# Performance work log

Measured on AMD Instinct MI355X. Metric: run time of the kernel, lower is better.

The kernel has to match this reference:

```python
import jax, jax.numpy as jnp
import numpy as np

TWO_PI = 2.0 * np.pi
EPS = 1e-6


def fourier_embed(x, W):
    # Gaussian Fourier features: x (B,L,1), W (1,F) -> (B,L,2F)
    p = TWO_PI * (x @ W)
    return jnp.concatenate([jnp.sin(p), jnp.cos(p)], axis=-1)


def phi(x, proj):
    # Stable positive softmax kernel (FAVOR+ eq. 7): exp(x W^T - |x|^2/2)/sqrt(m)
    m = proj.shape[0]
    xp = jnp.einsum('blhd,md->blhm', x, proj)
    h = 0.5 * jnp.sum(jnp.square(x), axis=-1, keepdims=True)
    return jnp.exp(xp - h) / jnp.sqrt(m)


def setup_inputs() -> dict:
    key = jax.random.key(0)
    kq, kk, kv, kqs, kks, kw, kp, ka = jax.random.split(key, 8)
    B, L, H, D, Dv = 4, 4096, 8, 64, 64
    M, S = 256, 64  # num_ortho_features, s_embd_dim
    return {
        'qs': jax.random.normal(kq, (B, L, H, D), jnp.float32),
        'ks': jax.random.normal(kk, (B, L, H, D), jnp.float32),
        'vs': jax.random.normal(kv, (B, L, H, Dv), jnp.float32),
        'qs_s': jax.random.uniform(kqs, (B, L, 1), jnp.float32),
        'ks_s': jax.random.uniform(kks, (B, L, 1), jnp.float32),
        'fourier_W': jax.random.normal(kw, (1, S // 2), jnp.float32),
        'qk_proj': jax.random.normal(kp, (M, D + S // H), jnp.float32),
        'a': jax.random.normal(ka, (1, 1, H, 1), jnp.float32),
    }


def reference(qs, ks, vs, qs_s, ks_s, fourier_W, qk_proj, a):
    B, Q, H, D = qs.shape
    K = ks.shape[1]
    S = 2 * fourier_W.shape[1]
    Dsh = S // H  # D_S_H

    # distance-bias projections, reshaped per-head; 'a' scales the query side
    qs_s_prime = a * fourier_embed(qs_s, fourier_W).reshape(B, Q, H, Dsh)
    ks_s_prime = fourier_embed(ks_s, fourier_W).reshape(B, K, H, Dsh)

    normalizer = D ** -0.25
    qs_prime = phi(jnp.concatenate([qs * normalizer, qs_s_prime], axis=-1), qk_proj)  # (B,Q,H,M)
    ks_prime = phi(jnp.concatenate([ks * normalizer, ks_s_prime], axis=-1), qk_proj)  # (B,K,H,M)

    # fast_attend: linear attention, never materializes QK^T
    c = jnp.concatenate([vs, jnp.ones((B, K, H, 1), vs.dtype)], axis=-1)  # (B,K,H,Dv+1)
    buf_1 = jnp.einsum('bkhm,bkhe->bhme', ks_prime, c)                    # (B,H,M,Dv+1)
    buf_2 = jnp.einsum('bqhm,bhme->bqhe', qs_prime, buf_1)                # (B,Q,H,Dv+1)
    num, den = buf_2[..., :-1], buf_2[..., -1]
    den = jnp.where(den < EPS, EPS, den)
    return num / den[..., None]  # (B,Q,H,Dv)
```

## Files before the change

### kernel.cpp

```cpp
#include <hip/hip_runtime.h>
#include <hip/hip_bf16.h>
#include <math.h>

#define BB 4
#define LLEN 4096
#define HH 8
#define MM 256
#define KX 96
#define EE 80
#define NTOK 16384
#define NORM 0.35355339059327373f
#define NORM2 0.125f
#define LN16 2.7725887222397811f
#define EPSV 1e-6f
#define TWO_PI_F 6.283185307179586f
#define NSPLIT 8

typedef __attribute__((ext_vector_type(8))) short s16x8;
typedef __attribute__((ext_vector_type(4))) short s16x4;
typedef __attribute__((ext_vector_type(4))) float f32x4;
typedef __attribute__((ext_vector_type(4))) unsigned int u32x4;

#define MFMA16(A,B,C) __builtin_amdgcn_mfma_f32_16x16x32_bf16(A,B,C,0,0,0)

static __device__ __forceinline__ unsigned short f2bf(float f) {
  union { float f; unsigned int u; } v; v.f = f;
  unsigned int r = v.u + 0x7FFFu + ((v.u >> 16) & 1u);
  return (unsigned short)(r >> 16);
}
static __device__ __forceinline__ unsigned int pk2(float lo, float hi) {
  __hip_bfloat162 h = __float22bfloat162_rn(make_float2(lo, hi));
  union { __hip_bfloat162 h; unsigned int u; } c; c.h = h;
  return c.u;
}

#define OFF_PROJF 0u
#define OFF_VF    524288u
#define OFF_PARTS (OFF_VF + 20971520u)
#define OFF_B1F   (OFF_PARTS + 41943040u)

__global__ __launch_bounds__(256) void prep_vF(const float* __restrict__ vs,
                                               const float* __restrict__ proj,
                                               unsigned short* __restrict__ vF,
                                               unsigned short* __restrict__ projF) {
  int kc = blockIdx.x;
  int bh = blockIdx.y;
  if (kc == 64) {
    if (bh != 0) return;
    int t = threadIdx.x;
    int l = t & 63, grp = t >> 6;
    int l15 = l & 15, l4 = l >> 4;
    for (int c = grp; c < 48; c += 4) {
      int mt = c / 3, xs = c % 3;
      int m = l15 + 16 * mt;
      s16x8 o;
#pragma unroll
      for (int j = 0; j < 8; ++j) {
        int d = 32 * xs + 8 * l4 + j;
        unsigned short u;
        if (d < 64)       u = f2bf(proj[m * 72 + d] * NORM);
        else if (d < 72)  u = f2bf(proj[m * 72 + d]);
        else if (d == 72) u = 0xBF80;
        else              u = 0;
        o[j] = (short)u;
      }
      *reinterpret_cast<s16x8*>(projF + ((size_t)c * 64 + l) * 8) = o;
    }
    return;
  }
  int b = bh >> 3, h = bh & 7;
  int t = threadIdx.x;
  __shared__ unsigned short tile[64][72];
  int k = t >> 2, seg = t & 3;
  const f32x4* src = reinterpret_cast<const f32x4*>(
      vs + (((size_t)(b * LLEN + kc * 64 + k)) * HH + h) * 64 + seg * 16);
#pragma unroll
  for (int j = 0; j < 4; ++j) {
    f32x4 v = src[j];
#pragma unroll
    for (int i = 0; i < 4; ++i) tile[k][seg * 16 + j * 4 + i] = f2bf(v[i]);
  }
  __syncthreads();
  int l = t & 63, ks2 = (t >> 6) & 1, rep = t >> 7;
  int l15 = l & 15, l4 = l >> 4;
  int nelo = rep ? 3 : 0, nehi = rep ? 5 : 3;
  for (int ne = nelo; ne < nehi; ++ne) {
    int e = l15 + 16 * ne;
    s16x8 o;
#pragma unroll
    for (int j = 0; j < 8; ++j) {
      int kl = 32 * ks2 + 16 * (j >> 2) + 4 * l4 + (j & 3);
      unsigned short u;
      if (e < 64)       u = tile[kl][e];
      else if (e == 64) u = 0x3F80;
      else              u = 0;
      o[j] = (short)u;
    }
    size_t kslot = (size_t)kc * 2 + ks2;
    *reinterpret_cast<s16x8*>(
        vF + (((size_t)bh * 128 + kslot) * 5 + ne) * 64 * 8 + (size_t)l * 8) = o;
  }
}

__global__ __launch_bounds__(1024, 1) void f1_k(
    const float* __restrict__ ks, const float* __restrict__ ks_s,
    const float* __restrict__ W,
    const unsigned short* __restrict__ projF,
    const unsigned short* __restrict__ vF,
    float* __restrict__ parts) {
  __shared__ unsigned short pf_lds[24576];
  __shared__ unsigned char  sbuf[2][13312];
  __shared__ alignas(16) float hk_sh[2][32];

  int bh = blockIdx.x, split = blockIdx.y;
  int b = bh >> 3, h = bh & 7;
  int tid = threadIdx.x;
  int w = tid >> 6, l = tid & 63;
  int l15 = l & 15, l4 = l >> 4;
  int kbase = split * 512;
  int row = tid >> 4, seg = tid & 15;
  int s4 = (row & 7) << 4;

  const float* ksb = ks + ((size_t)(b * LLEN + kbase) * HH + h) * 64;
  const float* kss = ks_s + (size_t)b * LLEN + kbase;
  const unsigned short* vfb = vF + ((size_t)bh * 128 + split * 16) * 5 * 64 * 8;

  float wv = 0.f; bool issin = false;
  if (seg < 8) { int dim = 8 * h + seg; wv = W[dim & 31] * TWO_PI_F; issin = dim < 32; }

  {
    if (tid < 512) {
      int bi = tid >> 8, rem = tid & 255;
      u32x4 z = {};
      *reinterpret_cast<u32x4*>(&sbuf[bi][(rem >> 3) * 256 + 128 + (rem & 7) * 16]) = z;
    }
    const u32x4* g1 = reinterpret_cast<const u32x4*>(projF);
    u32x4* s1 = reinterpret_cast<u32x4*>(pf_lds);
#pragma unroll
    for (int i = 0; i < 3; ++i) s1[i * 1024 + tid] = g1[i * 1024 + tid];
  }
  __syncthreads();
  if (tid < 512) {
    f32x4 kv = *reinterpret_cast<const f32x4*>(ksb + (size_t)row * 512 + 4 * seg);
    float part = (kv[0]*kv[0] + kv[1]*kv[1] + kv[2]*kv[2] + kv[3]*kv[3]) * NORM2;
    s16x4 o;
#pragma unroll
    for (int i = 0; i < 4; ++i) o[i] = (short)f2bf(kv[i]);
    *reinterpret_cast<s16x4*>(&sbuf[0][row * 256 + ((8 * seg) ^ s4)]) = o;
    if (seg < 8) {
      float ph = kss[row] * wv;
      float e = issin ? sinf(ph) : cosf(ph);
      part += e * e;
      *reinterpret_cast<unsigned short*>(&sbuf[0][row * 256 + ((128 + 2 * seg) ^ s4)]) = f2bf(e);
    }
#pragma unroll
    for (int m = 1; m < 16; m <<= 1) part += __shfl_xor(part, m, 64);
    if (seg == 0) hk_sh[0][row] = 0.5f * part + LN16;
  }
  if (tid < 320)
    *reinterpret_cast<u32x4*>(&sbuf[0][8192 + tid * 16]) =
        reinterpret_cast<const u32x4*>(vfb)[tid];
  __syncthreads();

  f32x4 acc2[5] = {};

  for (int it = 0; it < 16; ++it) {
    int cur = it & 1, nxt = cur ^ 1;
    f32x4 kvn; float svn = 0.f; u32x4 nv;
    if (it < 15) {
      if (tid < 512) {
        kvn = *reinterpret_cast<const f32x4*>(
            ksb + (size_t)(32 * (it + 1) + row) * 512 + 4 * seg);
        if (seg < 8) svn = kss[32 * (it + 1) + row];
      }
      if (tid < 320)
        nv = reinterpret_cast<const u32x4*>(vfb + (size_t)(it + 1) * 2560)[tid];
    }

    f32x4 acc1_0 = {}, acc1_1 = {};
#pragma unroll
    for (int xs = 0; xs < 3; ++xs) {
      int co = (64 * xs + 16 * l4) ^ ((l15 & 7) << 4);
      s16x8 ak0 = *reinterpret_cast<const s16x8*>(&sbuf[cur][l15 * 256 + co]);
      s16x8 ak1 = *reinterpret_cast<const s16x8*>(&sbuf[cur][(16 + l15) * 256 + co]);
      s16x8 pf = *reinterpret_cast<const s16x8*>(pf_lds + ((w * 3 + xs) * 64 + l) * 8);
      acc1_0 = MFMA16(ak0, pf, acc1_0);
      acc1_1 = MFMA16(ak1, pf, acc1_1);
    }
    f32x4 hk0 = *reinterpret_cast<const f32x4*>(&hk_sh[cur][4 * l4]);
    f32x4 hk1 = *reinterpret_cast<const f32x4*>(&hk_sh[cur][16 + 4 * l4]);
    union { unsigned int u[4]; s16x8 s; } P;
    P.u[0] = pk2(__expf(acc1_0[0] - hk0[0]), __expf(acc1_0[1] - hk0[1]));
    P.u[1] = pk2(__expf(acc1_0[2] - hk0[2]), __expf(acc1_0[3] - hk0[3]));
    P.u[2] = pk2(__expf(acc1_1[0] - hk1[0]), __expf(acc1_1[1] - hk1[1]));
    P.u[3] = pk2(__expf(acc1_1[2] - hk1[2]), __expf(acc1_1[3] - hk1[3]));
#pragma unroll
    for (int ne = 0; ne < 5; ++ne) {
      s16x8 vb = *reinterpret_cast<const s16x8*>(&sbuf[cur][8192 + (ne * 64 + l) * 16]);
      acc2[ne] = MFMA16(P.s, vb, acc2[ne]);
    }
    if (it < 15) {
      if (tid < 512) {
        float part = (kvn[0]*kvn[0] + kvn[1]*kvn[1] + kvn[2]*kvn[2] + kvn[3]*kvn[3]) * NORM2;
        s16x4 o;
#pragma unroll
        for (int i = 0; i < 4; ++i) o[i] = (short)f2bf(kvn[i]);
        *reinterpret_cast<s16x4*>(&sbuf[nxt][row * 256 + ((8 * seg) ^ s4)]) = o;
        if (seg < 8) {
          float ph = svn * wv;
          float e = issin ? sinf(ph) : cosf(ph);
          part += e * e;
          *reinterpret_cast<unsigned short*>(&sbuf[nxt][row * 256 + ((128 + 2 * seg) ^ s4)]) = f2bf(e);
        }
#pragma unroll
        for (int m = 1; m < 16; m <<= 1) part += __shfl_xor(part, m, 64);
        if (seg == 0) hk_sh[nxt][row] = 0.5f * part + LN16;
      }
      if (tid < 320) *reinterpret_cast<u32x4*>(&sbuf[nxt][8192 + tid * 16]) = nv;
    }
    __syncthreads();
  }

#pragma unroll
  for (int ne = 0; ne < 5; ++ne)
#pragma unroll
    for (int r = 0; r < 4; ++r) {
      int m = 16 * w + 4 * l4 + r;
      parts[(((size_t)split * 32 + bh) * MM + m) * EE + l15 + 16 * ne] = acc2[ne][r];
    }
}

__global__ __launch_bounds__(256) void reduce_t(const float* __restrict__ parts,
                                                unsigned short* __restrict__ b1F) {
  int bh = blockIdx.x;
  int mc = blockIdx.y;
  __shared__ float s[64 * 80];
  size_t base = ((size_t)bh * MM + mc * 64) * EE;
  for (int o = threadIdx.x; o < 64 * 80; o += 256) {
    float sum = 0.f;
#pragma unroll
    for (int sp = 0; sp < NSPLIT; ++sp)
      sum += parts[(size_t)sp * 32 * MM * EE + base + o];
    s[o] = sum;
  }
  __syncthreads();
  int t = threadIdx.x, l = t & 63, kl = (t >> 6) & 1, rep = t >> 7;
  int l15 = l & 15, l4 = l >> 4;
  int nelo = rep ? 3 : 0, nehi = rep ? 5 : 3;
  for (int ne = nelo; ne < nehi; ++ne) {
    s16x8 o;
#pragma unroll
    for (int j = 0; j < 8; ++j) {
      int ml = 32 * kl + 16 * (j >> 2) + 4 * l4 + (j & 3);
      o[j] = (short)f2bf(s[ml * 80 + l15 + 16 * ne]);
    }
    int ks = mc * 2 + kl;
    *reinterpret_cast<s16x8*>(
        b1F + (((size_t)bh * 8 + ks) * 5 + ne) * 64 * 8 + (size_t)l * 8) = o;
  }
}

__global__ __launch_bounds__(1024, 1) void f2_k(
    const float* __restrict__ qs, const float* __restrict__ qs_s,
    const float* __restrict__ W, const float* __restrict__ a,
    const unsigned short* __restrict__ projF,
    const unsigned short* __restrict__ b1F, float* __restrict__ out) {
  __shared__ unsigned short pf_lds[24576];
  __shared__ unsigned short b1_lds[20480];

  int bh = blockIdx.x, qc = blockIdx.y;
  int b = bh >> 3, h = bh & 7;
  int tid = threadIdx.x;
  int w = tid >> 6, l = tid & 63;
  int l15 = l & 15, l4 = l >> 4;
  int qb = qc * 512 + w * 32;
  const unsigned short* b1b = b1F + (size_t)bh * 8 * 5 * 64 * 8;
  float ah = a[h];

  {
    const u32x4* g1 = reinterpret_cast<const u32x4*>(projF);
    u32x4* s1 = reinterpret_cast<u32x4*>(pf_lds);
#pragma unroll
    for (int i = 0; i < 3; ++i) s1[i * 1024 + tid] = g1[i * 1024 + tid];
    const u32x4* g2 = reinterpret_cast<const u32x4*>(b1b);
    u32x4* s2 = reinterpret_cast<u32x4*>(b1_lds);
    s2[tid] = g2[tid];
    s2[1024 + tid] = g2[1024 + tid];
    if (tid < 512) s2[2048 + tid] = g2[2048 + tid];
  }

  s16x8 xq[2][3];
#pragma unroll
  for (int qt = 0; qt < 2; ++qt) {
    int qrow = qb + 16 * qt + l15;
    const float* qr = qs + ((size_t)(b * LLEN + qrow) * HH + h) * 64;
    float part = 0.f;
#pragma unroll
    for (int xs = 0; xs < 2; ++xs) {
      f32x4 u0 = *reinterpret_cast<const f32x4*>(qr + 32 * xs + 8 * l4);
      f32x4 u1 = *reinterpret_cast<const f32x4*>(qr + 32 * xs + 8 * l4 + 4);
      s16x8 fr;
#pragma unroll
      for (int i = 0; i < 4; ++i) {
        part += u0[i] * u0[i] + u1[i] * u1[i];
        fr[i] = (short)f2bf(u0[i]);
        fr[4 + i] = (short)f2bf(u1[i]);
      }
      xq[qt][xs] = fr;
    }
    part *= NORM2;
    s16x8 fx = {};
    if (l4 == 0) {
      float sv = qs_s[(size_t)b * LLEN + qrow] * TWO_PI_F;
#pragma unroll
      for (int j = 0; j < 8; ++j) {
        int dim = 8 * h + j;
        float ph = sv * W[dim & 31];
        float e = (dim < 32) ? sinf(ph) : cosf(ph);
        e *= ah;
        part += e * e;
        fx[j] = (short)f2bf(e);
      }
    }
    part += __shfl_xor(part, 16, 64);
    part += __shfl_xor(part, 32, 64);
    if (l4 == 1) fx[0] = (short)f2bf(0.5f * part + LN16);
    xq[qt][2] = fx;
  }
  __syncthreads();

  f32x4 acc3[2][5] = {};
#pragma unroll
  for (int ks = 0; ks < 8; ++ks) {
    f32x4 a0 = {}, b0 = {}, a1 = {}, b1 = {};
    __builtin_amdgcn_s_setprio(1);
#pragma unroll
    for (int xs = 0; xs < 3; ++xs) {
      s16x8 p0 = *reinterpret_cast<const s16x8*>(pf_lds + (((2 * ks) * 3 + xs) * 64 + l) * 8);
      s16x8 p1 = *reinterpret_cast<const s16x8*>(pf_lds + (((2 * ks + 1) * 3 + xs) * 64 + l) * 8);
      a0 = MFMA16(p0, xq[0][xs], a0);
      b0 = MFMA16(p1, xq[0][xs], b0);
      a1 = MFMA16(p0, xq[1][xs], a1);
      b1 = MFMA16(p1, xq[1][xs], b1);
    }
    __builtin_amdgcn_s_setprio(0);
    union { unsigned int u[4]; s16x8 s; } Pa, Pb;
    Pa.u[0] = pk2(__expf(a0[0]), __expf(a0[1]));
    Pa.u[1] = pk2(__expf(a0[2]), __expf(a0[3]));
    Pa.u[2] = pk2(__expf(b0[0]), __expf(b0[1]));
    Pa.u[3] = pk2(__expf(b0[2]), __expf(b0[3]));
    Pb.u[0] = pk2(__expf(a1[0]), __expf(a1[1]));
    Pb.u[1] = pk2(__expf(a1[2]), __expf(a1[3]));
    Pb.u[2] = pk2(__expf(b1[0]), __expf(b1[1]));
    Pb.u[3] = pk2(__expf(b1[2]), __expf(b1[3]));
    __builtin_amdgcn_s_setprio(1);
#pragma unroll
    for (int ne = 0; ne < 5; ++ne) {
      s16x8 vb = *reinterpret_cast<const s16x8*>(b1_lds + ((ks * 5 + ne) * 64 + l) * 8);
      acc3[0][ne] = MFMA16(Pa.s, vb, acc3[0][ne]);
      acc3[1][ne] = MFMA16(Pb.s, vb, acc3[1][ne]);
    }
    __builtin_amdgcn_s_setprio(0);
  }
#pragma unroll
  for (int qt = 0; qt < 2; ++qt) {
    float inv[4];
#pragma unroll
    for (int r = 0; r < 4; ++r) {
      float den = __shfl(acc3[qt][4][r], 16 * l4, 64);
      den = den < EPSV ? EPSV : den;
      inv[r] = 1.0f / den;
    }
#pragma unroll
    for (int ne = 0; ne < 4; ++ne)
#pragma unroll
      for (int r = 0; r < 4; ++r)
        out[((size_t)(b * LLEN + qb + 16 * qt + 4 * l4 + r) * HH + h) * 64 + l15 + 16 * ne] =
            acc3[qt][ne][r] * inv[r];
  }
}

extern "C" void kernel_launch(void* const* d_in, const int* in_sizes, int n_in,
                              void* d_out, int out_size, void* d_ws, size_t ws_size,
                              hipStream_t stream) {
  const float* qs   = (const float*)d_in[0];
  const float* ks   = (const float*)d_in[1];
  const float* vs   = (const float*)d_in[2];
  const float* qs_s = (const float*)d_in[3];
  const float* ks_s = (const float*)d_in[4];
  const float* W    = (const float*)d_in[5];
  const float* proj = (const float*)d_in[6];
  const float* a    = (const float*)d_in[7];
  float* out = (float*)d_out;

  char* ws = (char*)d_ws;
  unsigned short* projF = (unsigned short*)(ws + OFF_PROJF);
  unsigned short* vF    = (unsigned short*)(ws + OFF_VF);
  float*          parts = (float*)(ws + OFF_PARTS);
  unsigned short* b1F   = (unsigned short*)(ws + OFF_B1F);

  prep_vF<<<dim3(65, 32), 256, 0, stream>>>(vs, proj, vF, projF);
  f1_k<<<dim3(32, NSPLIT), 1024, 0, stream>>>(ks, ks_s, W, projF, vF, parts);
  reduce_t<<<dim3(32, 4), 256, 0, stream>>>(parts, b1F);
  f2_k<<<dim3(32, 8), 1024, 0, stream>>>(qs, qs_s, W, a, projF, b1F, out);
}
```

Measured before the change: 79.40 us.

## Fuse V conversion into f1 kernel using LDS transpose reads

Drops the separate prep pass that converted V to a bf16 fragment layout in global memory. f1_k now loads fp32 V directly, packs it to bf16 in LDS, and uses ds_read_b64_tr_b16 to read transposed MFMA operands. The ones-column for the denominator comes from a constant register fragment. This saves a full V read/write round trip and most of a launch, but adds inline asm with an explicit waitcnt and more global loads inside the main loop.

```diff
diff --git a/kernel.cpp b/kernel.cpp
--- a/kernel.cpp
+++ b/kernel.cpp
@@ -33,83 +33,47 @@
   union { __hip_bfloat162 h; unsigned int u; } c; c.h = h;
   return c.u;
 }
+static __device__ __forceinline__ s16x8 cat4(s16x4 a, s16x4 b) {
+  s16x8 r;
+  r[0]=a[0]; r[1]=a[1]; r[2]=a[2]; r[3]=a[3];
+  r[4]=b[0]; r[5]=b[1]; r[6]=b[2]; r[7]=b[3];
+  return r;
+}
 
 #define OFF_PROJF 0u
-#define OFF_VF    524288u
-#define OFF_PARTS (OFF_VF + 20971520u)
-#define OFF_B1F   (OFF_PARTS + 41943040u)
-
-__global__ __launch_bounds__(256) void prep_vF(const float* __restrict__ vs,
-                                               const float* __restrict__ proj,
-                                               unsigned short* __restrict__ vF,
-                                               unsigned short* __restrict__ projF) {
-  int kc = blockIdx.x;
-  int bh = blockIdx.y;
-  if (kc == 64) {
-    if (bh != 0) return;
-    int t = threadIdx.x;
-    int l = t & 63, grp = t >> 6;
-    int l15 = l & 15, l4 = l >> 4;
-    for (int c = grp; c < 48; c += 4) {
-      int mt = c / 3, xs = c % 3;
-      int m = l15 + 16 * mt;
-      s16x8 o;
-#pragma unroll
-      for (int j = 0; j < 8; ++j) {
-        int d = 32 * xs + 8 * l4 + j;
-        unsigned short u;
-        if (d < 64)       u = f2bf(proj[m * 72 + d] * NORM);
-        else if (d < 72)  u = f2bf(proj[m * 72 + d]);
-        else if (d == 72) u = 0xBF80;
-        else              u = 0;
-        o[j] = (short)u;
-      }
-      *reinterpret_cast<s16x8*>(projF + ((size_t)c * 64 + l) * 8) = o;
-    }
-    return;
-  }
-  int b = bh >> 3, h = bh & 7;
+#define OFF_PARTS 524288u
+#define OFF_B1F   (OFF_PARTS + 20971520u)
+
+__global__ __launch_bounds__(256) void prep_projF(const float* __restrict__ proj,
+                                                  unsigned short* __restrict__ projF) {
   int t = threadIdx.x;
-  __shared__ unsigned short tile[64][72];
-  int k = t >> 2, seg = t & 3;
-  const f32x4* src = reinterpret_cast<const f32x4*>(
-      vs + (((size_t)(b * LLEN + kc * 64 + k)) * HH + h) * 64 + seg * 16);
-#pragma unroll
-  for (int j = 0; j < 4; ++j) {
-    f32x4 v = src[j];
-#pragma unroll
-    for (int i = 0; i < 4; ++i) tile[k][seg * 16 + j * 4 + i] = f2bf(v[i]);
-  }
-  __syncthreads();
-  int l = t & 63, ks2 = (t >> 6) & 1, rep = t >> 7;
+  int l = t & 63, grp = t >> 6;
   int l15 = l & 15, l4 = l >> 4;
-  int nelo = rep ? 3 : 0, nehi = rep ? 5 : 3;
-  for (int ne = nelo; ne < nehi; ++ne) {
-    int e = l15 + 16 * ne;
+  for (int c = grp; c < 48; c += 4) {
+    int mt = c / 3, xs = c % 3;
+    int m = l15 + 16 * mt;
     s16x8 o;
 #pragma unroll
     for (int j = 0; j < 8; ++j) {
-      int kl = 32 * ks2 + 16 * (j >> 2) + 4 * l4 + (j & 3);
+      int d = 32 * xs + 8 * l4 + j;
       unsigned short u;
-      if (e < 64)       u = tile[kl][e];
-      else if (e == 64) u = 0x3F80;
+      if (d < 64)       u = f2bf(proj[m * 72 + d] * NORM);
+      else if (d < 72)  u = f2bf(proj[m * 72 + d]);
+      else if (d == 72) u = 0xBF80;
       else              u = 0;
       o[j] = (short)u;
     }
-    size_t kslot = (size_t)kc * 2 + ks2;
-    *reinterpret_cast<s16x8*>(
-        vF + (((size_t)bh * 128 + kslot) * 5 + ne) * 64 * 8 + (size_t)l * 8) = o;
+    *reinterpret_cast<s16x8*>(projF + ((size_t)c * 64 + l) * 8) = o;
   }
 }
 
 __global__ __launch_bounds__(1024, 1) void f1_k(
     const float* __restrict__ ks, const float* __restrict__ ks_s,
-    const float* __restrict__ W,
+    const float* __restrict__ vs, const float* __restrict__ W,
     const unsigned short* __restrict__ projF,
-    const unsigned short* __restrict__ vF,
     float* __restrict__ parts) {
   __shared__ unsigned short pf_lds[24576];
-  __shared__ unsigned char  sbuf[2][13312];
+  __shared__ alignas(16) unsigned char sbuf[2][12288];
   __shared__ alignas(16) float hk_sh[2][32];
 
   int bh = blockIdx.x, split = blockIdx.y;
@@ -122,18 +86,20 @@
   int s4 = (row & 7) << 4;
 
   const float* ksb = ks + ((size_t)(b * LLEN + kbase) * HH + h) * 64;
+  const float* vsb = vs + ((size_t)(b * LLEN + kbase) * HH + h) * 64;
   const float* kss = ks_s + (size_t)b * LLEN + kbase;
-  const unsigned short* vfb = vF + ((size_t)bh * 128 + split * 16) * 5 * 64 * 8;
 
   float wv = 0.f; bool issin = false;
   if (seg < 8) { int dim = 8 * h + seg; wv = W[dim & 31] * TWO_PI_F; issin = dim < 32; }
 
+  int vwo = 8192 + (seg >> 2) * 1024 + row * 32 + (seg & 3) * 8;
+
+  if (tid < 512) {
+    int bi = tid >> 8, rem = tid & 255;
+    u32x4 z = {};
+    *reinterpret_cast<u32x4*>(&sbuf[bi][(rem >> 3) * 256 + 128 + (rem & 7) * 16]) = z;
+  }
   {
-    if (tid < 512) {
-      int bi = tid >> 8, rem = tid & 255;
-      u32x4 z = {};
-      *reinterpret_cast<u32x4*>(&sbuf[bi][(rem >> 3) * 256 + 128 + (rem & 7) * 16]) = z;
-    }
     const u32x4* g1 = reinterpret_cast<const u32x4*>(projF);
     u32x4* s1 = reinterpret_cast<u32x4*>(pf_lds);
 #pragma unroll
@@ -156,25 +122,27 @@
 #pragma unroll
     for (int m = 1; m < 16; m <<= 1) part += __shfl_xor(part, m, 64);
     if (seg == 0) hk_sh[0][row] = 0.5f * part + LN16;
-  }
-  if (tid < 320)
-    *reinterpret_cast<u32x4*>(&sbuf[0][8192 + tid * 16]) =
-        reinterpret_cast<const u32x4*>(vfb)[tid];
+    f32x4 vv = *reinterpret_cast<const f32x4*>(vsb + (size_t)row * 512 + 4 * seg);
+    uint2 vp = make_uint2(pk2(vv[0], vv[1]), pk2(vv[2], vv[3]));
+    *reinterpret_cast<uint2*>(&sbuf[0][vwo]) = vp;
+  }
   __syncthreads();
+
+  s16x8 vb4 = {};
+  if (l15 == 0) {
+#pragma unroll
+    for (int j = 0; j < 8; ++j) vb4[j] = (short)0x3F80;
+  }
 
   f32x4 acc2[5] = {};
 
   for (int it = 0; it < 16; ++it) {
     int cur = it & 1, nxt = cur ^ 1;
-    f32x4 kvn; float svn = 0.f; u32x4 nv;
-    if (it < 15) {
-      if (tid < 512) {
-        kvn = *reinterpret_cast<const f32x4*>(
-            ksb + (size_t)(32 * (it + 1) + row) * 512 + 4 * seg);
-        if (seg < 8) svn = kss[32 * (it + 1) + row];
-      }
-      if (tid < 320)
-        nv = reinterpret_cast<const u32x4*>(vfb + (size_t)(it + 1) * 2560)[tid];
+    f32x4 kvn, vvn; float svn = 0.f;
+    if (it < 15 && tid < 512) {
+      kvn = *reinterpret_cast<const f32x4*>(ksb + (size_t)(32 * (it + 1) + row) * 512 + 4 * seg);
+      vvn = *reinterpret_cast<const f32x4*>(vsb + (size_t)(32 * (it + 1) + row) * 512 + 4 * seg);
+      if (seg < 8) svn = kss[32 * (it + 1) + row];
     }
 
     f32x4 acc1_0 = {}, acc1_1 = {};
@@ -194,29 +162,48 @@
     P.u[1] = pk2(__expf(acc1_0[2] - hk0[2]), __expf(acc1_0[3] - hk0[3]));
     P.u[2] = pk2(__expf(acc1_1[0] - hk1[0]), __expf(acc1_1[1] - hk1[1]));
     P.u[3] = pk2(__expf(acc1_1[2] - hk1[2]), __expf(acc1_1[3] - hk1[3]));
-#pragma unroll
-    for (int ne = 0; ne < 5; ++ne) {
-      s16x8 vb = *reinterpret_cast<const s16x8*>(&sbuf[cur][8192 + (ne * 64 + l) * 16]);
-      acc2[ne] = MFMA16(P.s, vb, acc2[ne]);
-    }
-    if (it < 15) {
-      if (tid < 512) {
-        float part = (kvn[0]*kvn[0] + kvn[1]*kvn[1] + kvn[2]*kvn[2] + kvn[3]*kvn[3]) * NORM2;
-        s16x4 o;
-#pragma unroll
-        for (int i = 0; i < 4; ++i) o[i] = (short)f2bf(kvn[i]);
-        *reinterpret_cast<s16x4*>(&sbuf[nxt][row * 256 + ((8 * seg) ^ s4)]) = o;
-        if (seg < 8) {
-          float ph = svn * wv;
-          float e = issin ? sinf(ph) : cosf(ph);
-          part += e * e;
-          *reinterpret_cast<unsigned short*>(&sbuf[nxt][row * 256 + ((128 + 2 * seg) ^ s4)]) = f2bf(e);
-        }
-#pragma unroll
-        for (int m = 1; m < 16; m <<= 1) part += __shfl_xor(part, m, 64);
-        if (seg == 0) hk_sh[nxt][row] = 0.5f * part + LN16;
+
+    unsigned int va = (unsigned int)(size_t)(&sbuf[cur][8192]) + 8 * l15 + 128 * l4;
+    s16x4 t0, t1, t2, t3, t4, t5, t6, t7;
+    asm volatile(
+        "ds_read_b64_tr_b16 %0, %8 offset:0\n\t"
+        "ds_read_b64_tr_b16 %1, %8 offset:512\n\t"
+        "ds_read_b64_tr_b16 %2, %8 offset:1024\n\t"
+        "ds_read_b64_tr_b16 %3, %8 offset:1536\n\t"
+        "ds_read_b64_tr_b16 %4, %8 offset:2048\n\t"
+        "ds_read_b64_tr_b16 %5, %8 offset:2560\n\t"
+        "ds_read_b64_tr_b16 %6, %8 offset:3072\n\t"
+        "ds_read_b64_tr_b16 %7, %8 offset:3584"
+        : "=&v"(t0), "=&v"(t1), "=&v"(t2), "=&v"(t3),
+          "=&v"(t4), "=&v"(t5), "=&v"(t6), "=&v"(t7)
+        : "v"(va)
+        : "memory");
+    asm volatile("s_waitcnt lgkmcnt(0)" ::: "memory");
+    __builtin_amdgcn_sched_barrier(0);
+
+    acc2[0] = MFMA16(P.s, cat4(t0, t1), acc2[0]);
+    acc2[1] = MFMA16(P.s, cat4(t2, t3), acc2[1]);
+    acc2[2] = MFMA16(P.s, cat4(t4, t5), acc2[2]);
+    acc2[3] = MFMA16(P.s, cat4(t6, t7), acc2[3]);
+    acc2[4] = MFMA16(P.s, vb4, acc2[4]);
+
+    if (it < 15 && tid < 512) {
+      float part = (kvn[0]*kvn[0] + kvn[1]*kvn[1] + kvn[2]*kvn[2] + kvn[3]*kvn[3]) * NORM2;
+      s16x4 o;
+#pragma unroll
+      for (int i = 0; i < 4; ++i) o[i] = (short)f2bf(kvn[i]);
+      *reinterpret_cast<s16x4*>(&sbuf[nxt][row * 256 + ((8 * seg) ^ s4)]) = o;
+      if (seg < 8) {
+        float ph = svn * wv;
+        float e = issin ? sinf(ph) : cosf(ph);
+        part += e * e;
+        *reinterpret_cast<unsigned short*>(&sbuf[nxt][row * 256 + ((128 + 2 * seg) ^ s4)]) = f2bf(e);
       }
-      if (tid < 320) *reinterpret_cast<u32x4*>(&sbuf[nxt][8192 + tid * 16]) = nv;
+#pragma unroll
+      for (int m = 1; m < 16; m <<= 1) part += __shfl_xor(part, m, 64);
+      if (seg == 0) hk_sh[nxt][row] = 0.5f * part + LN16;
+      uint2 vp = make_uint2(pk2(vvn[0], vvn[1]), pk2(vvn[2], vvn[3]));
+      *reinterpret_cast<uint2*>(&sbuf[nxt][vwo]) = vp;
     }
     __syncthreads();
   }
@@ -395,12 +382,11 @@
 
   char* ws = (char*)d_ws;
   unsigned short* projF = (unsigned short*)(ws + OFF_PROJF);
-  unsigned short* vF    = (unsigned short*)(ws + OFF_VF);
   float*          parts = (float*)(ws + OFF_PARTS);
   unsigned short* b1F   = (unsigned short*)(ws + OFF_B1F);
 
-  prep_vF<<<dim3(65, 32), 256, 0, stream>>>(vs, proj, vF, projF);
-  f1_k<<<dim3(32, NSPLIT), 1024, 0, stream>>>(ks, ks_s, W, projF, vF, parts);
+  prep_projF<<<1, 256, 0, stream>>>(proj, projF);
+  f1_k<<<dim3(32, NSPLIT), 1024, 0, stream>>>(ks, ks_s, vs, W, projF, parts);
   reduce_t<<<dim3(32, 4), 256, 0, stream>>>(parts, b1F);
   f2_k<<<dim3(32, 8), 1024, 0, stream>>>(qs, qs_s, W, a, projF, b1F, out);
 }
```

New measurement: 73.79 us, median of 2. 1.08x faster.
